# Kernel tuning notes

Measured on AMD Instinct MI355X. Metric: run time of the kernel, lower is better.

Reference implementation:

```python
import jax, jax.numpy as jnp
import numpy as np

TOP_K = 2


def setup_inputs() -> dict:
    key = jax.random.key(0)
    k1, k2 = jax.random.split(key)
    hidden_states = jax.random.normal(k1, (4, 8192, 4096), dtype=jnp.float32)
    # xavier_uniform for Linear(4096 -> 64): bound = sqrt(6/(fan_in+fan_out))
    bound = float(np.sqrt(6.0 / (4096 + 64)))
    gate_w = jax.random.uniform(k2, (64, 4096), dtype=jnp.float32, minval=-bound, maxval=bound)
    return {"hidden_states": hidden_states, "gate_w": gate_w}


def reference(hidden_states, gate_w):
    # Flatten [B, S, H] -> [T, H]
    H = hidden_states.shape[-1]
    x = hidden_states.reshape(-1, H)
    # Gate projection: [T, H] @ [H, E] -> [T, E]
    router_logits = jnp.einsum('th,eh->te', x, gate_w)
    # Top-k expert selection (eval mode: no noise)
    top_k_logits, top_k_indices = jax.lax.top_k(router_logits, TOP_K)
    # Normalize selected weights with a softmax over the k logits
    top_k_weights = jax.nn.softmax(top_k_logits, axis=-1)
    return top_k_weights, top_k_indices, router_logits
```

## Files before the change

kernel.cpp:

```cpp
#include <hip/hip_runtime.h>


#define NT    256
#define TT    32768
#define HD    4096
#define NE    64
#define NST   64
#define BUFB  16384u
#define NBUF  3

typedef __attribute__((ext_vector_type(8))) short bf16x8;
typedef __attribute__((ext_vector_type(4))) float f32x4;

#define MFMA __builtin_amdgcn_mfma_f32_16x16x32_bf16

__device__ __forceinline__ bf16x8 u2b(uint4 u) { return __builtin_bit_cast(bf16x8, u); }
__device__ __forceinline__ float4 b4f(uint4 u) { return __builtin_bit_cast(float4, u); }

__device__ __forceinline__ void gload_lds16(const void* g, void* l) {
  __builtin_amdgcn_global_load_lds(
      (const __attribute__((address_space(1))) void*)g,
      (__attribute__((address_space(3))) void*)l, 16, 0, 0);
}

__device__ __forceinline__ void tsplit8(float4 a, float4 b,
                                        uint4& o0, uint4& o1, uint4& o2) {
  float f[8] = {a.x, a.y, a.z, a.w, b.x, b.y, b.z, b.w};
  unsigned p0[4], p1[4], p2[4];
#pragma unroll
  for (int j = 0; j < 4; ++j) {
    float x0 = f[2 * j], x1 = f[2 * j + 1];
    unsigned u0 = __float_as_uint(x0) & 0xffff0000u;
    unsigned u1 = __float_as_uint(x1) & 0xffff0000u;
    float r0 = x0 - __uint_as_float(u0);
    float r1 = x1 - __uint_as_float(u1);
    unsigned v0 = __float_as_uint(r0) & 0xffff0000u;
    unsigned v1 = __float_as_uint(r1) & 0xffff0000u;
    float s0 = r0 - __uint_as_float(v0);
    float s1 = r1 - __uint_as_float(v1);
    p0[j] = (u0 >> 16) | u1;
    p1[j] = (v0 >> 16) | v1;
    p2[j] = (__float_as_uint(s0) >> 16) | (__float_as_uint(s1) & 0xffff0000u);
  }
  o0 = make_uint4(p0[0], p0[1], p0[2], p0[3]);
  o1 = make_uint4(p1[0], p1[1], p1[2], p1[3]);
  o2 = make_uint4(p2[0], p2[1], p2[2], p2[3]);
}

__global__ __launch_bounds__(256)
void prepack_w_kernel(const float* __restrict__ W, uint4* __restrict__ Bp) {
  const int t  = blockIdx.x * 256 + threadIdx.x;
  const int e  = t >> 9;
  const int k0 = (t & 511) * 8;
  const float4* wp = (const float4*)(W + (size_t)e * HD + k0);
  uint4 o0, o1, o2;
  tsplit8(wp[0], wp[1], o0, o1, o2);
  const int ts = k0 >> 5;
  const int lg = (k0 >> 3) & 3;
  const int f  = e >> 4;
  const int ln = lg * 16 + (e & 15);
  Bp[(((ts * 3 + 0) * 4 + f) << 6) + ln] = o0;
  Bp[(((ts * 3 + 1) * 4 + f) << 6) + ln] = o1;
  Bp[(((ts * 3 + 2) * 4 + f) << 6) + ln] = o2;
}

#define PROD1(AM0, AM1, BN0, BN1) \
    acc00 = MFMA(AM0, BN0, acc00, 0, 0, 0); \
    acc01 = MFMA(AM0, BN1, acc01, 0, 0, 0); \
    acc10 = MFMA(AM1, BN0, acc10, 0, 0, 0); \
    acc11 = MFMA(AM1, BN1, acc11, 0, 0, 0);

__global__ __launch_bounds__(NT, 2)
void router_pipe_kernel(const float* __restrict__ A, const uint4* __restrict__ Bp,
                        float* __restrict__ outw, float* __restrict__ outi,
                        float* __restrict__ outl) {
  __shared__ __align__(16) unsigned char smem[NBUF * BUFB];

  const int tid  = threadIdx.x;
  const int bm   = blockIdx.x;
  const int lane = tid & 63;
  const int w    = tid >> 6;
  const int wr   = w >> 1;
  const int wc   = w & 1;
  const int l15  = lane & 15;
  const int lg   = lane >> 4;
  const int x7   = l15 & 7;

  const char* Ab = (const char*)A;

  unsigned soff[4];
#pragma unroll
  for (int j = 0; j < 4; ++j) {
    int rj = w * 16 + j * 4 + lg;
    int gs = l15 ^ (rj & 7);
    soff[j] = (unsigned)((bm * 64 + rj) * (HD * 4)) + (unsigned)(gs * 16);
  }

#define DMA(T, BD) { \
    const int tc_ = (T) > (NST - 1) ? (NST - 1) : (T); \
    _Pragma("unroll") \
    for (int j = 0; j < 4; ++j) \
      gload_lds16(Ab + (size_t)soff[j] + (size_t)tc_ * 256, \
                  smem + (BD) + (unsigned)((w * 4 + j) * 1024)); }

  const uint4* pbB = Bp + wc * 128 + lane;

#define LOADB(P, T) { \
    const int tc_ = (T) > (NST - 1) ? (NST - 1) : (T); \
    const uint4* q_ = pbB + (size_t)tc_ * 1536; \
    P##s0L0f0 = q_[0];    P##s0L0f1 = q_[64]; \
    P##s0L1f0 = q_[256];  P##s0L1f1 = q_[320]; \
    P##s0L2f0 = q_[512];  P##s0L2f1 = q_[576]; \
    P##s1L0f0 = q_[768];  P##s1L0f1 = q_[832]; \
    P##s1L1f0 = q_[1024]; P##s1L1f1 = q_[1088]; \
    P##s1L2f0 = q_[1280]; P##s1L2f1 = q_[1344]; }

  uint4 Es0L0f0, Es0L0f1, Es0L1f0, Es0L1f1, Es0L2f0, Es0L2f1;
  uint4 Es1L0f0, Es1L0f1, Es1L1f0, Es1L1f1, Es1L2f0, Es1L2f1;
  uint4 Os0L0f0, Os0L0f1, Os0L1f0, Os0L1f1, Os0L2f0, Os0L2f1;
  uint4 Os1L0f0, Os1L0f1, Os1L1f0, Os1L1f1, Os1L2f0, Os1L2f1;

  f32x4 acc00 = {0.f,0.f,0.f,0.f}, acc01 = {0.f,0.f,0.f,0.f};
  f32x4 acc10 = {0.f,0.f,0.f,0.f}, acc11 = {0.f,0.f,0.f,0.f};

  const unsigned r0base = (unsigned)((wr * 32 + l15) * 256);

#define BSTEPX(BC, S, B0f0, B0f1, B1f0, B1f1, B2f0, B2f1) { \
    const int gi_ = (S) * 8 + lg * 2; \
    const unsigned glo_ = (unsigned)((gi_ ^ x7) << 4); \
    const unsigned ghi_ = (unsigned)(((gi_ + 1) ^ x7) << 4); \
    const unsigned char* b0_ = smem + (BC) + r0base; \
    const unsigned char* b1_ = b0_ + 16 * 256; \
    uint4 a0lo = *(const uint4*)(b0_ + glo_); \
    uint4 a0hi = *(const uint4*)(b0_ + ghi_); \
    uint4 a1lo = *(const uint4*)(b1_ + glo_); \
    uint4 a1hi = *(const uint4*)(b1_ + ghi_); \
    uint4 x0_, x1_, x2_, y0_, y1_, y2_; \
    tsplit8(b4f(a0lo), b4f(a0hi), x0_, x1_, x2_); \
    tsplit8(b4f(a1lo), b4f(a1hi), y0_, y1_, y2_); \
    const bf16x8 a0m0 = u2b(x0_), a1m0 = u2b(x1_), a2m0 = u2b(x2_); \
    const bf16x8 a0m1 = u2b(y0_), a1m1 = u2b(y1_), a2m1 = u2b(y2_); \
    PROD1(a0m0, a0m1, u2b(B2f0), u2b(B2f1)) \
    PROD1(a1m0, a1m1, u2b(B1f0), u2b(B1f1)) \
    PROD1(a2m0, a2m1, u2b(B0f0), u2b(B0f1)) \
    PROD1(a0m0, a0m1, u2b(B1f0), u2b(B1f1)) \
    PROD1(a1m0, a1m1, u2b(B0f0), u2b(B0f1)) \
    PROD1(a0m0, a0m1, u2b(B0f0), u2b(B0f1)) }

#define COMPUTE2(BC, P) \
    BSTEPX(BC, 0, P##s0L0f0, P##s0L0f1, P##s0L1f0, P##s0L1f1, P##s0L2f0, P##s0L2f1) \
    BSTEPX(BC, 1, P##s1L0f0, P##s1L0f1, P##s1L1f0, P##s1L1f1, P##s1L2f0, P##s1L2f1)

#define HALF(ST, LOADSET, COMPSET) { \
    asm volatile("s_waitcnt vmcnt(16)" ::: "memory"); \
    __builtin_amdgcn_s_barrier(); \
    __builtin_amdgcn_sched_barrier(0); \
    LOADB(LOADSET, (ST) + 1) \
    DMA((ST) + 2, bd) \
    __builtin_amdgcn_sched_barrier(0); \
    COMPUTE2(bc, COMPSET) \
    bc += BUFB; if (bc == NBUF * BUFB) bc = 0; \
    bd += BUFB; if (bd == NBUF * BUFB) bd = 0; }

  DMA(0, 0u)
  asm volatile("" ::: "memory");
  LOADB(E, 0)
  DMA(1, BUFB)

  unsigned bc = 0, bd = 2 * BUFB;

#pragma unroll 1
  for (int p = 0; p < NST / 2; ++p) {
    HALF(2 * p,     O, E)
    HALF(2 * p + 1, E, O)
  }

  asm volatile("s_waitcnt vmcnt(0)" ::: "memory");
  __syncthreads();

  const int t0 = bm * 64;
  float* lf = (float*)smem;

#define EPO(MI, NI, ACC) \
  { _Pragma("unroll") \
    for (int r = 0; r < 4; ++r) { \
      int tl = wr * 32 + (MI) * 16 + lg * 4 + r; \
      int e  = wc * 32 + (NI) * 16 + l15; \
      float v = ACC[r]; \
      outl[(size_t)(t0 + tl) * NE + e] = v; \
      lf[tl * 65 + e] = v; \
    } }
  EPO(0, 0, acc00) EPO(0, 1, acc01) EPO(1, 0, acc10) EPO(1, 1, acc11)
#undef EPO

  __syncthreads();

  if (tid < 64) {
    const int t = tid;
    float m1 = -1e30f, m2 = -1e30f;
    int i1 = 0, i2 = 0;
#pragma unroll
    for (int e = 0; e < NE; ++e) {
      float v = lf[t * 65 + e];
      if (v > m1)      { m2 = m1; i2 = i1; m1 = v; i1 = e; }
      else if (v > m2) { m2 = v; i2 = e; }
    }
    float e2  = expf(m2 - m1);
    float inv = 1.0f / (1.0f + e2);
    outw[(size_t)(t0 + t) * 2 + 0] = inv;
    outw[(size_t)(t0 + t) * 2 + 1] = e2 * inv;
    outi[(size_t)(t0 + t) * 2 + 0] = (float)i1;
    outi[(size_t)(t0 + t) * 2 + 1] = (float)i2;
  }
}

__global__ __launch_bounds__(256, 2)
void topk_router_lds(const float* __restrict__ A, const float* __restrict__ W,
                     float* __restrict__ outw, float* __restrict__ outi,
                     float* __restrict__ outl) {
  __shared__ __align__(16) unsigned char smem[49152];
  const int tid  = threadIdx.x;
  const int bm   = blockIdx.x;
  const int lane = tid & 63;
  const int wid  = tid >> 6;
  const int wr   = wid >> 1;
  const int wc   = wid & 1;
  const int l15  = lane & 15;
  const int lg   = lane >> 4;
  const int s_r  = tid >> 2;
  const int s_cb = (tid & 3) << 3;
  const float* aball = A + (size_t)(bm * 64 + s_r) * HD + s_cb;
  const float* bball = W + (size_t)s_r * HD + s_cb;
  const unsigned wswz  = ((unsigned)((s_r >> 1) & 3)) << 4;
  const unsigned wbyte = (unsigned)(s_r * 64) + (((unsigned)(s_cb * 2)) ^ wswz);
  f32x4 acc00 = {0.f,0.f,0.f,0.f}, acc01 = {0.f,0.f,0.f,0.f};
  f32x4 acc10 = {0.f,0.f,0.f,0.f}, acc11 = {0.f,0.f,0.f,0.f};
  float4 aE0, aE1, bE0, bE1, aO0, aO1, bO0, bO1;
#define LOADS(T, A0, A1, B0, B1) { \
    const float4* ap = (const float4*)(aball + (size_t)(T) * 32); \
    A0 = ap[0]; A1 = ap[1]; \
    const float4* bp = (const float4*)(bball + (size_t)(T) * 32); \
    B0 = bp[0]; B1 = bp[1]; }
#define CONVW2(BB, A0, A1, B0, B1) { \
    uint4 o0, o1, o2; \
    tsplit8(A0, A1, o0, o1, o2); \
    *(uint4*)(smem + (BB) +     0 + wbyte) = o0; \
    *(uint4*)(smem + (BB) +  4096 + wbyte) = o1; \
    *(uint4*)(smem + (BB) +  8192 + wbyte) = o2; \
    tsplit8(B0, B1, o0, o1, o2); \
    *(uint4*)(smem + (BB) + 12288 + wbyte) = o0; \
    *(uint4*)(smem + (BB) + 16384 + wbyte) = o1; \
    *(uint4*)(smem + (BB) + 20480 + wbyte) = o2; }
  auto compute = [&](int bb) {
    bf16x8 a0m0, a0m1, a1m0, a1m1, a2m0, a2m1;
    bf16x8 b0n0, b0n1, b1n0, b1n1, b2n0, b2n1;
    const unsigned kb = (unsigned)(lg * 16);
#define LDA(SI, MI, DST) { \
    int row = wr * 32 + (MI) * 16 + l15; \
    DST = *(const bf16x8*)(smem + bb + (SI) * 4096 + row * 64 + \
          (kb ^ ((((unsigned)row >> 1) & 3) << 4))); }
#define LDB(SI, NI, DST) { \
    int row = wc * 32 + (NI) * 16 + l15; \
    DST = *(const bf16x8*)(smem + bb + 12288 + (SI) * 4096 + row * 64 + \
          (kb ^ ((((unsigned)row >> 1) & 3) << 4))); }
    LDA(0, 0, a0m0) LDA(0, 1, a0m1)
    LDA(1, 0, a1m0) LDA(1, 1, a1m1)
    LDA(2, 0, a2m0) LDA(2, 1, a2m1)
    LDB(0, 0, b0n0) LDB(0, 1, b0n1)
    LDB(1, 0, b1n0) LDB(1, 1, b1n1)
    LDB(2, 0, b2n0) LDB(2, 1, b2n1)
#undef LDA
#undef LDB
    PROD1(a0m0, a0m1, b2n0, b2n1)
    PROD1(a1m0, a1m1, b1n0, b1n1)
    PROD1(a2m0, a2m1, b0n0, b0n1)
    PROD1(a0m0, a0m1, b1n0, b1n1)
    PROD1(a1m0, a1m1, b0n0, b0n1)
    PROD1(a0m0, a0m1, b0n0, b0n1)
  };
  LOADS(0, aE0, aE1, bE0, bE1)
  LOADS(1, aO0, aO1, bO0, bO1)
  CONVW2(0, aE0, aE1, bE0, bE1)
  __syncthreads();
#pragma unroll 1
  for (int kk = 0; kk < 128; kk += 2) {
    if (kk + 2 < 128) { LOADS(kk + 2, aE0, aE1, bE0, bE1) }
    __builtin_amdgcn_sched_barrier(0);
    compute(0);
    CONVW2(24576, aO0, aO1, bO0, bO1)
    __syncthreads();
    if (kk + 3 < 128) { LOADS(kk + 3, aO0, aO1, bO0, bO1) }
    __builtin_amdgcn_sched_barrier(0);
    compute(24576);
    if (kk + 2 < 128) { CONVW2(0, aE0, aE1, bE0, bE1) }
    __syncthreads();
  }
  const int t0 = bm * 64;
  float* lf2 = (float*)smem;
#define EPI(MI, NI, ACC) \
  { _Pragma("unroll") \
    for (int r = 0; r < 4; ++r) { \
      int tl = wr * 32 + (MI) * 16 + lg * 4 + r; \
      int e  = wc * 32 + (NI) * 16 + l15; \
      float v = ACC[r]; \
      outl[(size_t)(t0 + tl) * NE + e] = v; \
      lf2[tl * 65 + e] = v; \
    } }
  EPI(0, 0, acc00) EPI(0, 1, acc01) EPI(1, 0, acc10) EPI(1, 1, acc11)
#undef EPI
  __syncthreads();
  if (tid < 64) {
    const int t = tid;
    float m1 = -1e30f, m2 = -1e30f;
    int i1 = 0, i2 = 0;
#pragma unroll
    for (int e = 0; e < NE; ++e) {
      float v = lf2[t * 65 + e];
      if (v > m1)      { m2 = m1; i2 = i1; m1 = v; i1 = e; }
      else if (v > m2) { m2 = v; i2 = e; }
    }
    float e2  = expf(m2 - m1);
    float inv = 1.0f / (1.0f + e2);
    outw[(size_t)(t0 + t) * 2 + 0] = inv;
    outw[(size_t)(t0 + t) * 2 + 1] = e2 * inv;
    outi[(size_t)(t0 + t) * 2 + 0] = (float)i1;
    outi[(size_t)(t0 + t) * 2 + 1] = (float)i2;
  }
}

extern "C" void kernel_launch(void* const* d_in, const int* in_sizes, int n_in,
                              void* d_out, int out_size, void* d_ws, size_t ws_size,
                              hipStream_t stream) {
  (void)in_sizes; (void)n_in; (void)out_size;
  const float* A = (const float*)d_in[0];
  const float* W = (const float*)d_in[1];
  float* outw = (float*)d_out;
  float* outi = (float*)d_out + 2 * TT;
  float* outl = (float*)d_out + 4 * TT;

  const size_t need = (size_t)128 * 3 * 4 * 1024;
  if (ws_size >= need) {
    hipLaunchKernelGGL(prepack_w_kernel, dim3(128), dim3(256), 0, stream,
                       W, (uint4*)d_ws);
    hipLaunchKernelGGL(router_pipe_kernel, dim3(TT / 64), dim3(NT), 0, stream,
                       A, (const uint4*)d_ws, outw, outi, outl);
  } else {
    hipLaunchKernelGGL(topk_router_lds, dim3(TT / 64), dim3(256), 0, stream,
                       A, W, outw, outi, outl);
  }
}
```

Measured before the change: 170.3 us.

## Restructure router GEMM into 32-row blocks with double-buffered 32KB pages

Replaces the 64-row, 256-thread, triple-buffered pipeline with a 512-thread kernel in which each block handles 32 tokens. Eight waves each own a 16x16 output tile, and the kernel streams A through two 32KB LDS pages, each covering 256 columns. B fragments are loaded just-in-time per step instead of being prefetched into registers. The aim is more blocks, higher occupancy and fewer registers, with fewer barriers per K. In exchange, each wave gets less MFMA reuse per A load, B is re-read from global/L2 more often, and vmcnt(0) waits leave less overlap between loading and compute.

```diff
diff --git a/kernel.cpp b/kernel.cpp
--- a/kernel.cpp
+++ b/kernel.cpp
@@ -1,13 +1,13 @@
 #include <hip/hip_runtime.h>
 
 
-#define NT    256
+#define NT    512
 #define TT    32768
 #define HD    4096
 #define NE    64
-#define NST   64
-#define BUFB  16384u
-#define NBUF  3
+#define MROWS 32
+#define NSUP  16
+#define BUFB  32768u
 
 typedef __attribute__((ext_vector_type(8))) short bf16x8;
 typedef __attribute__((ext_vector_type(4))) float f32x4;
@@ -64,138 +64,97 @@
   Bp[(((ts * 3 + 2) * 4 + f) << 6) + ln] = o2;
 }
 
-#define PROD1(AM0, AM1, BN0, BN1) \
-    acc00 = MFMA(AM0, BN0, acc00, 0, 0, 0); \
-    acc01 = MFMA(AM0, BN1, acc01, 0, 0, 0); \
-    acc10 = MFMA(AM1, BN0, acc10, 0, 0, 0); \
-    acc11 = MFMA(AM1, BN1, acc11, 0, 0, 0);
-
-__global__ __launch_bounds__(NT, 2)
-void router_pipe_kernel(const float* __restrict__ A, const uint4* __restrict__ Bp,
+__global__ __launch_bounds__(NT, 4)
+void router_page_kernel(const float* __restrict__ A, const uint4* __restrict__ Bp,
                         float* __restrict__ outw, float* __restrict__ outi,
                         float* __restrict__ outl) {
-  __shared__ __align__(16) unsigned char smem[NBUF * BUFB];
+  __shared__ __align__(16) unsigned char smem[65536];
 
   const int tid  = threadIdx.x;
   const int bm   = blockIdx.x;
   const int lane = tid & 63;
   const int w    = tid >> 6;
-  const int wr   = w >> 1;
-  const int wc   = w & 1;
+  const int wm   = w >> 2;
+  const int wn   = w & 3;
   const int l15  = lane & 15;
   const int lg   = lane >> 4;
-  const int x7   = l15 & 7;
+  const unsigned key = (unsigned)(l15 & 7);
 
   const char* Ab = (const char*)A;
 
-  unsigned soff[4];
+  unsigned soff[4], ldst[4];
 #pragma unroll
   for (int j = 0; j < 4; ++j) {
-    int rj = w * 16 + j * 4 + lg;
-    int gs = l15 ^ (rj & 7);
-    soff[j] = (unsigned)((bm * 64 + rj) * (HD * 4)) + (unsigned)(gs * 16);
-  }
-
-#define DMA(T, BD) { \
-    const int tc_ = (T) > (NST - 1) ? (NST - 1) : (T); \
+    const int r = w * 4 + j;
+    soff[j] = (unsigned)((bm * MROWS + r) * (HD * 4))
+            + (((unsigned)lane ^ ((unsigned)r & 7u)) << 4);
+    ldst[j] = (unsigned)(r * 1024);
+  }
+
+#define DMA(T, BOFF) { \
     _Pragma("unroll") \
     for (int j = 0; j < 4; ++j) \
-      gload_lds16(Ab + (size_t)soff[j] + (size_t)tc_ * 256, \
-                  smem + (BD) + (unsigned)((w * 4 + j) * 1024)); }
-
-  const uint4* pbB = Bp + wc * 128 + lane;
-
-#define LOADB(P, T) { \
-    const int tc_ = (T) > (NST - 1) ? (NST - 1) : (T); \
-    const uint4* q_ = pbB + (size_t)tc_ * 1536; \
-    P##s0L0f0 = q_[0];    P##s0L0f1 = q_[64]; \
-    P##s0L1f0 = q_[256];  P##s0L1f1 = q_[320]; \
-    P##s0L2f0 = q_[512];  P##s0L2f1 = q_[576]; \
-    P##s1L0f0 = q_[768];  P##s1L0f1 = q_[832]; \
-    P##s1L1f0 = q_[1024]; P##s1L1f1 = q_[1088]; \
-    P##s1L2f0 = q_[1280]; P##s1L2f1 = q_[1344]; }
-
-  uint4 Es0L0f0, Es0L0f1, Es0L1f0, Es0L1f1, Es0L2f0, Es0L2f1;
-  uint4 Es1L0f0, Es1L0f1, Es1L1f0, Es1L1f1, Es1L2f0, Es1L2f1;
-  uint4 Os0L0f0, Os0L0f1, Os0L1f0, Os0L1f1, Os0L2f0, Os0L2f1;
-  uint4 Os1L0f0, Os1L0f1, Os1L1f0, Os1L1f1, Os1L2f0, Os1L2f1;
-
-  f32x4 acc00 = {0.f,0.f,0.f,0.f}, acc01 = {0.f,0.f,0.f,0.f};
-  f32x4 acc10 = {0.f,0.f,0.f,0.f}, acc11 = {0.f,0.f,0.f,0.f};
-
-  const unsigned r0base = (unsigned)((wr * 32 + l15) * 256);
-
-#define BSTEPX(BC, S, B0f0, B0f1, B1f0, B1f1, B2f0, B2f1) { \
-    const int gi_ = (S) * 8 + lg * 2; \
-    const unsigned glo_ = (unsigned)((gi_ ^ x7) << 4); \
-    const unsigned ghi_ = (unsigned)(((gi_ + 1) ^ x7) << 4); \
-    const unsigned char* b0_ = smem + (BC) + r0base; \
-    const unsigned char* b1_ = b0_ + 16 * 256; \
-    uint4 a0lo = *(const uint4*)(b0_ + glo_); \
-    uint4 a0hi = *(const uint4*)(b0_ + ghi_); \
-    uint4 a1lo = *(const uint4*)(b1_ + glo_); \
-    uint4 a1hi = *(const uint4*)(b1_ + ghi_); \
-    uint4 x0_, x1_, x2_, y0_, y1_, y2_; \
-    tsplit8(b4f(a0lo), b4f(a0hi), x0_, x1_, x2_); \
-    tsplit8(b4f(a1lo), b4f(a1hi), y0_, y1_, y2_); \
-    const bf16x8 a0m0 = u2b(x0_), a1m0 = u2b(x1_), a2m0 = u2b(x2_); \
-    const bf16x8 a0m1 = u2b(y0_), a1m1 = u2b(y1_), a2m1 = u2b(y2_); \
-    PROD1(a0m0, a0m1, u2b(B2f0), u2b(B2f1)) \
-    PROD1(a1m0, a1m1, u2b(B1f0), u2b(B1f1)) \
-    PROD1(a2m0, a2m1, u2b(B0f0), u2b(B0f1)) \
-    PROD1(a0m0, a0m1, u2b(B1f0), u2b(B1f1)) \
-    PROD1(a1m0, a1m1, u2b(B0f0), u2b(B0f1)) \
-    PROD1(a0m0, a0m1, u2b(B0f0), u2b(B0f1)) }
-
-#define COMPUTE2(BC, P) \
-    BSTEPX(BC, 0, P##s0L0f0, P##s0L0f1, P##s0L1f0, P##s0L1f1, P##s0L2f0, P##s0L2f1) \
-    BSTEPX(BC, 1, P##s1L0f0, P##s1L0f1, P##s1L1f0, P##s1L1f1, P##s1L2f0, P##s1L2f1)
-
-#define HALF(ST, LOADSET, COMPSET) { \
-    asm volatile("s_waitcnt vmcnt(16)" ::: "memory"); \
-    __builtin_amdgcn_s_barrier(); \
-    __builtin_amdgcn_sched_barrier(0); \
-    LOADB(LOADSET, (ST) + 1) \
-    DMA((ST) + 2, bd) \
-    __builtin_amdgcn_sched_barrier(0); \
-    COMPUTE2(bc, COMPSET) \
-    bc += BUFB; if (bc == NBUF * BUFB) bc = 0; \
-    bd += BUFB; if (bd == NBUF * BUFB) bd = 0; }
+      gload_lds16(Ab + (size_t)soff[j] + (size_t)(T) * 1024, \
+                  smem + (BOFF) + ldst[j]); }
+
+  const uint4* pb = Bp + wn * 64 + lane;
+
+  const unsigned abase = (unsigned)((wm * 16 + l15) * 1024);
+
+  f32x4 acc = {0.f, 0.f, 0.f, 0.f};
+
+#define STEP(BOFF, G, S) { \
+    const uint4* q_ = pb + (size_t)(G) * 768; \
+    const uint4 b0_ = q_[0], b1_ = q_[256], b2_ = q_[512]; \
+    const unsigned g0_ = (unsigned)((S) * 8 + lg * 2); \
+    const unsigned char* ab_ = smem + (BOFF) + abase; \
+    const uint4 alo_ = *(const uint4*)(ab_ + ((g0_ ^ key) << 4)); \
+    const uint4 ahi_ = *(const uint4*)(ab_ + (((g0_ + 1) ^ key) << 4)); \
+    uint4 x0_, x1_, x2_; \
+    tsplit8(b4f(alo_), b4f(ahi_), x0_, x1_, x2_); \
+    const bf16x8 a0_ = u2b(x0_), a1_ = u2b(x1_), a2_ = u2b(x2_); \
+    acc = MFMA(a0_, u2b(b2_), acc, 0, 0, 0); \
+    acc = MFMA(a1_, u2b(b1_), acc, 0, 0, 0); \
+    acc = MFMA(a2_, u2b(b0_), acc, 0, 0, 0); \
+    acc = MFMA(a0_, u2b(b1_), acc, 0, 0, 0); \
+    acc = MFMA(a1_, u2b(b0_), acc, 0, 0, 0); \
+    acc = MFMA(a0_, u2b(b0_), acc, 0, 0, 0); }
 
   DMA(0, 0u)
-  asm volatile("" ::: "memory");
-  LOADB(E, 0)
-  DMA(1, BUFB)
-
-  unsigned bc = 0, bd = 2 * BUFB;
-
+
+  unsigned cb = 0;
 #pragma unroll 1
-  for (int p = 0; p < NST / 2; ++p) {
-    HALF(2 * p,     O, E)
-    HALF(2 * p + 1, E, O)
-  }
-
-  asm volatile("s_waitcnt vmcnt(0)" ::: "memory");
+  for (int t = 0; t < NSUP; ++t) {
+    asm volatile("s_waitcnt vmcnt(0)" ::: "memory");
+    __builtin_amdgcn_s_barrier();
+    __builtin_amdgcn_sched_barrier(0);
+    if (t + 1 < NSUP) { DMA(t + 1, cb ^ BUFB) }
+    __builtin_amdgcn_sched_barrier(0);
+    const int g0 = t * 8;
+    STEP(cb, g0 + 0, 0) STEP(cb, g0 + 1, 1)
+    STEP(cb, g0 + 2, 2) STEP(cb, g0 + 3, 3)
+    STEP(cb, g0 + 4, 4) STEP(cb, g0 + 5, 5)
+    STEP(cb, g0 + 6, 6) STEP(cb, g0 + 7, 7)
+    cb ^= BUFB;
+  }
+
+  const int t0 = bm * MROWS;
+  float* lf = (float*)smem;
+
+  {
+    const int e = wn * 16 + l15;
+#pragma unroll
+    for (int r = 0; r < 4; ++r) {
+      const int row = wm * 16 + lg * 4 + r;
+      const float v = acc[r];
+      outl[(size_t)(t0 + row) * NE + e] = v;
+      lf[row * 65 + e] = v;
+    }
+  }
+
   __syncthreads();
 
-  const int t0 = bm * 64;
-  float* lf = (float*)smem;
-
-#define EPO(MI, NI, ACC) \
-  { _Pragma("unroll") \
-    for (int r = 0; r < 4; ++r) { \
-      int tl = wr * 32 + (MI) * 16 + lg * 4 + r; \
-      int e  = wc * 32 + (NI) * 16 + l15; \
-      float v = ACC[r]; \
-      outl[(size_t)(t0 + tl) * NE + e] = v; \
-      lf[tl * 65 + e] = v; \
-    } }
-  EPO(0, 0, acc00) EPO(0, 1, acc01) EPO(1, 0, acc10) EPO(1, 1, acc11)
-#undef EPO
-
-  __syncthreads();
-
-  if (tid < 64) {
+  if (tid < MROWS) {
     const int t = tid;
     float m1 = -1e30f, m2 = -1e30f;
     int i1 = 0, i2 = 0;
@@ -213,6 +172,12 @@
     outi[(size_t)(t0 + t) * 2 + 1] = (float)i2;
   }
 }
+
+#define PROD1(AM0, AM1, BS0, BS1) \
+    acc00 = MFMA(AM0, BS0, acc00, 0, 0, 0); \
+    acc01 = MFMA(AM0, BS1, acc01, 0, 0, 0); \
+    acc10 = MFMA(AM1, BS0, acc10, 0, 0, 0); \
+    acc11 = MFMA(AM1, BS1, acc11, 0, 0, 0);
 
 __global__ __launch_bounds__(256, 2)
 void topk_router_lds(const float* __restrict__ A, const float* __restrict__ W,
@@ -342,7 +307,7 @@
   if (ws_size >= need) {
     hipLaunchKernelGGL(prepack_w_kernel, dim3(128), dim3(256), 0, stream,
                        W, (uint4*)d_ws);
-    hipLaunchKernelGGL(router_pipe_kernel, dim3(TT / 64), dim3(NT), 0, stream,
+    hipLaunchKernelGGL(router_page_kernel, dim3(TT / MROWS), dim3(NT), 0, stream,
                        A, (const uint4*)d_ws, outw, outi, outl);
   } else {
     hipLaunchKernelGGL(topk_router_lds, dim3(TT / 64), dim3(256), 0, stream,
```

New measurement: 225.0 us. 1.32x slower.
